# Optimization experiments

Hardware: AMD Instinct MI355X
Metric: run time of the kernel (lower is better)

The kernel has to match this reference:

```python
import jax, jax.numpy as jnp
import numpy as np

BS, Hq, Wq = 4, 64, 64
C, M, K, L = 256, 8, 4, 4
CV = C // M
SCALES = [(64, 64), (32, 32), (16, 16), (8, 8)]


def grid_sample_nhwc(img, grid):
    """torch.F.grid_sample(mode='bilinear', padding_mode='zeros', align_corners=False).
    img: [N,h,w,Cf], grid: [N,H,W,2] with (x,y) in [-1,1]. Returns [N,H,W,Cf]."""
    N, h, w, _ = img.shape
    x = (grid[..., 0] + 1.0) * (w * 0.5) - 0.5
    y = (grid[..., 1] + 1.0) * (h * 0.5) - 0.5
    x0 = jnp.floor(x)
    y0 = jnp.floor(y)
    wx1 = x - x0
    wy1 = y - y0
    wx0 = 1.0 - wx1
    wy0 = 1.0 - wy1
    b = jnp.arange(N)[:, None, None]

    def gather(yi, xi):
        valid = ((xi >= 0) & (xi < w) & (yi >= 0) & (yi < h)).astype(img.dtype)
        xi_c = jnp.clip(xi, 0, w - 1).astype(jnp.int32)
        yi_c = jnp.clip(yi, 0, h - 1).astype(jnp.int32)
        return img[b, yi_c, xi_c] * valid[..., None]  # [N,H,W,Cf]

    return (gather(y0, x0) * (wy0 * wx0)[..., None]
            + gather(y0, x0 + 1.0) * (wy0 * wx1)[..., None]
            + gather(y0 + 1.0, x0) * (wy1 * wx0)[..., None]
            + gather(y0 + 1.0, x0 + 1.0) * (wy1 * wx1)[..., None])


def _forward(q, feats, ref, Wz, bz, Wo, bo, Wa, ba, Wp, bp, Wm, bm):
    BM = BS * M
    z = q @ Wz + bz  # [BS,H,W,C]
    # learned offsets: [BS,H,W,2MKL] -> [BS,M,L,K,H,W,2] -> [BM,L,K,H,W,2]
    off = (z @ Wo + bo).reshape(BS, Hq, Wq, M, L, K, 2)
    off = off.transpose(0, 3, 4, 5, 1, 2, 6).reshape(BM, L, K, Hq, Wq, 2)
    # attention weights over the L*K samples per head
    attn = jax.nn.softmax((z @ Wa + ba).reshape(BS, Hq, Wq, M, L * K), axis=-1)
    attn = attn.transpose(0, 3, 1, 2, 4).reshape(BM, Hq * Wq, L * K)

    samples = []
    for l, f in enumerate(feats):
        h, w = f.shape[1], f.shape[2]
        # value projection, split heads: [BS,h,w,C] -> [BM,h,w,CV] (BS outer, M inner)
        wp = (f @ Wp + bp).reshape(BS, h, w, M, CV).transpose(0, 3, 1, 2, 4).reshape(BM, h, w, CV)
        # phi(h,w,ref) then .repeat(M,1,1,1): tile with M as the OUTER axis (faithful to source)
        pref = jnp.stack([ref[..., 0] * (w - 1), ref[..., 1] * (h - 1)], axis=-1)  # [BS,H,W,2]
        pref = jnp.tile(pref, (M, 1, 1, 1))  # [BM,H,W,2]
        pts = pref[:, None] + off[:, l]  # [BM,K,H,W,2]
        gx = 2.0 * pts[..., 0] / max(w - 1, 1) - 1.0
        gy = 2.0 * pts[..., 1] / max(h - 1, 1) - 1.0
        grid = jnp.stack([gx, gy], axis=-1)  # [BM,K,H,W,2]
        s = jax.vmap(grid_sample_nhwc, in_axes=(None, 1), out_axes=0)(wp, grid)  # [K,BM,H,W,CV]
        samples.append(s.transpose(1, 4, 2, 0, 3))  # [BM,CV,H,K,W] == torch.stack(..., dim=3)

    sf = jnp.stack(samples, axis=1)  # [BM,L,CV,H,K,W]
    # faithful to source: permute(0,4,5,3,1,2) then raw view to [BM, H*W, CV, L*K]
    sf = sf.transpose(0, 4, 5, 3, 1, 2).reshape(BM, Hq * Wq, CV, L * K)
    out = jnp.einsum('nlds,nls->nld', sf, attn)  # [BM,HW,CV]
    out = out.reshape(BS, M, Hq, Wq, CV).transpose(0, 2, 3, 1, 4).reshape(BS, Hq, Wq, C)
    return out @ Wm + bm


def setup_inputs() -> dict:
    key = jax.random.key(0)
    ks = jax.random.split(key, 12)
    s = 0.02
    inp = {
        'q': jax.random.normal(ks[0], (BS, Hq, Wq, C), jnp.float32),
        'ref': jax.random.uniform(ks[1], (BS, Hq, Wq, 2), jnp.float32),
    }
    for i, (h, w) in enumerate(SCALES):
        inp[f'feat{i}'] = jax.random.normal(jax.random.fold_in(ks[2], i), (BS, h, w, C), jnp.float32)
    inp['Wz'] = jax.random.normal(ks[3], (C, C), jnp.float32) * s
    inp['bz'] = jnp.zeros((C,), jnp.float32)
    inp['Wo'] = jax.random.normal(ks[4], (C, 2 * M * K * L), jnp.float32) * s
    inp['bo'] = jnp.zeros((2 * M * K * L,), jnp.float32)
    inp['Wa'] = jax.random.normal(ks[5], (C, M * K * L), jnp.float32) * s
    inp['ba'] = jnp.zeros((M * K * L,), jnp.float32)
    inp['Wp'] = jax.random.normal(ks[6], (C, C), jnp.float32) * s
    inp['bp'] = jnp.zeros((C,), jnp.float32)
    inp['Wm'] = jax.random.normal(ks[7], (C, C), jnp.float32) * s
    inp['bm'] = jnp.zeros((C,), jnp.float32)
    return inp


def reference(q, feat0, feat1, feat2, feat3, ref, Wz, bz, Wo, bo, Wa, ba, Wp, bp, Wm, bm):
    return _forward(q, [feat0, feat1, feat2, feat3], ref, Wz, bz, Wo, bo, Wa, ba, Wp, bp, Wm, bm)
```

## Files before the change

### kernel.cpp

```cpp
#include <hip/hip_runtime.h>
#include <hip/hip_bf16.h>


typedef __attribute__((ext_vector_type(8))) _Float16 half8;
typedef __attribute__((ext_vector_type(2))) _Float16 half2t;
typedef __attribute__((ext_vector_type(4))) float f32x4;

#if __has_builtin(__builtin_amdgcn_fdot2)
__device__ __forceinline__ float fdot2f(half2t a, half2t b, float c) {
    return __builtin_amdgcn_fdot2(a, b, c, false);
}
#else
__device__ __forceinline__ float fdot2f(half2t a, half2t b, float c) {
    return c + (float)a.x * (float)b.x + (float)a.y * (float)b.y;
}
#endif

#define GLOAD_LDS16(gp, lp)                                                      \
    __builtin_amdgcn_global_load_lds(                                            \
        (const __attribute__((address_space(1))) void*)(gp),                     \
        (__attribute__((address_space(3))) void*)(lp), 16, 0, 0)

__device__ __forceinline__ int swz(int row, int sem_q) {
    return row * 32 + ((sem_q ^ (row & 3)) * 8);
}

__global__ __launch_bounds__(256) void transpose_w(
    const float* __restrict__ Wz, const float* __restrict__ Wo,
    const float* __restrict__ Wa, const float* __restrict__ Wp,
    const float* __restrict__ Wm,
    _Float16* __restrict__ Wzt, _Float16* __restrict__ Woat,
    _Float16* __restrict__ Wpt, _Float16* __restrict__ Wmt)
{
    __shared__ float ts[64][65];
    const int bid = blockIdx.x;
    const float* src; _Float16* dst; int N, tile;
    if      (bid < 16) { src = Wz; dst = Wzt;          N = 256; tile = bid; }
    else if (bid < 32) { src = Wo; dst = Woat;         N = 256; tile = bid - 16; }
    else if (bid < 40) { src = Wa; dst = Woat + 65536; N = 128; tile = bid - 32; }
    else if (bid < 56) { src = Wp; dst = Wpt;          N = 256; tile = bid - 40; }
    else               { src = Wm; dst = Wmt;          N = 256; tile = bid - 56; }
    const int ntn = N >> 6;
    const int k0 = (tile / ntn) * 64, n0 = (tile % ntn) * 64;
    const int t = threadIdx.x, tx = t & 63, ty = t >> 6;
    #pragma unroll
    for (int r = 0; r < 16; ++r) {
        const int kk = r * 4 + ty;
        ts[kk][tx] = src[(size_t)(k0 + kk) * N + n0 + tx];
    }
    __syncthreads();
    #pragma unroll
    for (int r = 0; r < 16; ++r) {
        const int nn = r * 4 + ty;
        dst[(size_t)(n0 + nn) * 256 + k0 + tx] = (_Float16)ts[tx][nn];
    }
}

template<typename AT>
__device__ __forceinline__ void gemm_core(
    _Float16* __restrict__ As, _Float16* __restrict__ Bs,
    const AT* __restrict__ A, const _Float16* __restrict__ Bt,
    int m0, int n0, f32x4 (&acc)[4][4])
{
    const int t    = threadIdx.x;
    const int lane = t & 63, wid = t >> 6;
    const int wr = wid >> 1, wc = wid & 1;
    const int lr = lane & 15, sq = lane >> 4;

    const int grow = lane >> 2;
    const int gqs  = (lane & 3) ^ ((lane >> 2) & 3);

    for (int kt = 0; kt < 256; kt += 32) {
        if constexpr (sizeof(AT) == 4) {
            const int arow = t >> 1, ac = t & 1;
            const float* ap = (const float*)A + (size_t)(m0 + arow) * 256 + kt + ac * 16;
            float v[16];
            #pragma unroll
            for (int i = 0; i < 4; ++i) {
                float4 f = ((const float4*)ap)[i];
                v[4*i] = f.x; v[4*i+1] = f.y; v[4*i+2] = f.z; v[4*i+3] = f.w;
            }
            half8 h0, h1;
            #pragma unroll
            for (int i = 0; i < 8; ++i) { h0[i] = (_Float16)v[i]; h1[i] = (_Float16)v[8+i]; }
            *(half8*)&As[swz(arow, ac * 2)]     = h0;
            *(half8*)&As[swz(arow, ac * 2 + 1)] = h1;
        } else {
            #pragma unroll
            for (int h = 0; h < 2; ++h) {
                const int rbase = wid * 32 + h * 16;
                const _Float16* ga = (const _Float16*)A +
                    (size_t)(m0 + rbase + grow) * 256 + kt + gqs * 8;
                GLOAD_LDS16(ga, &As[rbase * 32]);
            }
        }
        #pragma unroll
        for (int h = 0; h < 2; ++h) {
            const int rbase = wid * 32 + h * 16;
            const _Float16* gb = Bt +
                (size_t)(n0 + rbase + grow) * 256 + kt + gqs * 8;
            GLOAD_LDS16(gb, &Bs[rbase * 32]);
        }
        __syncthreads();

        half8 af[4], bf[4];
        #pragma unroll
        for (int m = 0; m < 4; ++m)
            af[m] = *(const half8*)&As[swz(wr*64 + m*16 + lr, sq)];
        #pragma unroll
        for (int n = 0; n < 4; ++n)
            bf[n] = *(const half8*)&Bs[swz(wc*64 + n*16 + lr, sq)];
        #pragma unroll
        for (int m = 0; m < 4; ++m)
            #pragma unroll
            for (int n = 0; n < 4; ++n)
                acc[m][n] = __builtin_amdgcn_mfma_f32_16x16x32_f16(af[m], bf[n], acc[m][n], 0, 0, 0);
        __syncthreads();
    }
}

__device__ __forceinline__ void epi_f16(
    f32x4 (&acc)[4][4], const float* __restrict__ bias,
    _Float16* __restrict__ C, int N, int m0, int n0)
{
    const int t = threadIdx.x, lane = t & 63, wid = t >> 6;
    const int wr = wid >> 1, wc = wid & 1, lr = lane & 15;
    #pragma unroll
    for (int n = 0; n < 4; ++n) {
        const int col = n0 + wc*64 + n*16 + lr;
        const float bv = bias[col];
        #pragma unroll
        for (int m = 0; m < 4; ++m)
            #pragma unroll
            for (int r = 0; r < 4; ++r) {
                const int row = m0 + wr*64 + m*16 + (lane >> 4)*4 + r;
                C[(size_t)row * N + col] = (_Float16)(acc[m][n][r] + bv);
            }
    }
}

__device__ __forceinline__ void epi_wp(
    f32x4 (&acc)[4][4], const float* __restrict__ bias,
    _Float16* __restrict__ C, int m0, int n0, int shift)
{
    const int t = threadIdx.x, lane = t & 63, wid = t >> 6;
    const int wr = wid >> 1, wc = wid & 1, lr = lane & 15;
    const int mask = (1 << shift) - 1;
    #pragma unroll
    for (int n = 0; n < 4; ++n) {
        const int col = n0 + wc*64 + n*16 + lr;
        const float bv = bias[col];
        const int mh = col >> 5, cv = col & 31;
        #pragma unroll
        for (int m = 0; m < 4; ++m)
            #pragma unroll
            for (int r = 0; r < 4; ++r) {
                const int row = m0 + wr*64 + m*16 + (lane >> 4)*4 + r;
                const int bb = row >> shift, pix = row & mask;
                C[((((size_t)(bb * 8 + mh)) << shift) + pix) * 32 + cv] =
                    (_Float16)(acc[m][n][r] + bv);
            }
    }
}

__global__ __launch_bounds__(256) void gemm_z_wp(
    const float* __restrict__ q, const _Float16* __restrict__ Wzt,
    const float* __restrict__ bz, _Float16* __restrict__ z,
    const float* __restrict__ f0, const float* __restrict__ f1,
    const float* __restrict__ f2, const float* __restrict__ f3,
    const _Float16* __restrict__ Wpt, const float* __restrict__ bp,
    _Float16* __restrict__ w0, _Float16* __restrict__ w1,
    _Float16* __restrict__ w2, _Float16* __restrict__ w3)
{
    __shared__ _Float16 As[128 * 32];
    __shared__ _Float16 Bs[128 * 32];
    const int by = blockIdx.y, bx = blockIdx.x;
    f32x4 acc[4][4] = {};
    if (by < 128) {
        gemm_core<float>(As, Bs, q, Wzt, by * 128, bx * 128, acc);
        epi_f16(acc, bz, z, 256, by * 128, bx * 128);
    } else {
        const int y = by - 128;
        const float* A; _Float16* C; int m0, shift;
        if      (y < 128) { A = f0; C = w0; m0 = y * 128;         shift = 12; }
        else if (y < 160) { A = f1; C = w1; m0 = (y - 128) * 128; shift = 10; }
        else if (y < 168) { A = f2; C = w2; m0 = (y - 160) * 128; shift = 8;  }
        else              { A = f3; C = w3; m0 = (y - 168) * 128; shift = 6;  }
        gemm_core<float>(As, Bs, A, Wpt, m0, bx * 128, acc);
        epi_wp(acc, bp, C, m0, bx * 128, shift);
    }
}

__global__ __launch_bounds__(256) void gemm_zo_at(
    const _Float16* __restrict__ z, const _Float16* __restrict__ Woat,
    const float* __restrict__ bo, const float* __restrict__ ba,
    _Float16* __restrict__ zo, _Float16* __restrict__ attn)
{
    __shared__ __align__(16) char ldsbuf[128 * 136 * 2];
    _Float16* As = (_Float16*)ldsbuf;
    _Float16* Bs = As + 128 * 32;
    _Float16 (*smax)[136] = (_Float16(*)[136])ldsbuf;

    const int bx = blockIdx.x, by = blockIdx.y;
    const int m0 = by * 128;
    f32x4 acc[4][4] = {};
    gemm_core<_Float16>(As, Bs, z, Woat, m0, bx * 128, acc);

    const int t = threadIdx.x, lane = t & 63, wid = t >> 6;
    const int wr = wid >> 1, wc = wid & 1, lr = lane & 15;

    if (bx < 2) {
        #pragma unroll
        for (int n = 0; n < 4; ++n) {
            const int c = bx * 128 + wc*64 + n*16 + lr;
            const float bv = bo[c];
            const int cp = (((c >> 3) & 3) << 6) | ((c >> 5) << 3)
                         | (((c >> 1) & 3) << 1) | (c & 1);
            #pragma unroll
            for (int m = 0; m < 4; ++m)
                #pragma unroll
                for (int r = 0; r < 4; ++r) {
                    const int row = m0 + wr*64 + m*16 + (lane >> 4)*4 + r;
                    zo[(size_t)row * 256 + cp] = (_Float16)(acc[m][n][r] + bv);
                }
        }
    } else {
        __syncthreads();
        #pragma unroll
        for (int n = 0; n < 4; ++n) {
            const int col = wc*64 + n*16 + lr;
            const float bv = ba[col];
            #pragma unroll
            for (int m = 0; m < 4; ++m)
                #pragma unroll
                for (int r = 0; r < 4; ++r) {
                    const int rowl = wr*64 + m*16 + (lane >> 4)*4 + r;
                    smax[rowl][col] = (_Float16)(acc[m][n][r] + bv);
                }
        }
        __syncthreads();
        #pragma unroll
        for (int j = 0; j < 4; ++j) {
            const int g    = j * 256 + t;
            const int rowl = g >> 3, mh = g & 7;
            const half8* sp = (const half8*)&smax[rowl][mh * 16];
            const half8 a = sp[0], bb8 = sp[1];
            float v[16];
            #pragma unroll
            for (int i = 0; i < 8; ++i) { v[i] = (float)a[i]; v[8+i] = (float)bb8[i]; }
            float mx = v[0];
            #pragma unroll
            for (int i = 1; i < 16; ++i) mx = fmaxf(mx, v[i]);
            float s = 0.f;
            #pragma unroll
            for (int i = 0; i < 16; ++i) { v[i] = expf(v[i] - mx); s += v[i]; }
            const float inv = 1.f / s;
            half8 o0, o1;
            #pragma unroll
            for (int i = 0; i < 8; ++i) { o0[i] = (_Float16)(v[i]*inv); o1[i] = (_Float16)(v[8+i]*inv); }
            const int row  = m0 + rowl;
            const int qpos = row & 4095, b = row >> 12;
            const int k = qpos >> 10, qx = (qpos >> 4) & 63, ya = qpos & 15;
            half8* op = (half8*)(attn +
                ((((((size_t)b * 64 + qx) * 16 + ya) * 8 + mh) * 4 + k) * 16));
            op[0] = o0; op[1] = o1;
        }
    }
}

__global__ __launch_bounds__(256) void sample8(
    const _Float16* __restrict__ zo,
    const _Float16* __restrict__ attn,
    const float* __restrict__ ref,
    const _Float16* __restrict__ wp0, const _Float16* __restrict__ wp1,
    const _Float16* __restrict__ wp2, const _Float16* __restrict__ wp3,
    _Float16* __restrict__ outp)
{
    const int bid = blockIdx.x;
    const int bp_ = (bid & 7) * 1024 + (bid >> 3);
    const int t  = threadIdx.x;
    const int k  = t & 3;
    const int m  = (t >> 2) & 7;
    const int qp = (t >> 5) & 1;
    const int l  = t >> 6;

    const int query = bp_ * 2 + qp;
    const int qx = query & 63;
    const int qy = (query >> 6) & 63;
    const int b  = query >> 12;

    const int ya = qy >> 2, yb = qy & 3;
    const int p  = (k << 10) | (qx << 4) | ya;
    const int cb = m * 32 + yb * 8 + l * 2;

    const int hw = 64 >> l;
    const int shift = 12 - 2 * l;
    const float fw = (float)hw;
    const _Float16* wp = (l == 0) ? wp0 : (l == 1) ? wp1 : (l == 2) ? wp2 : wp3;

    const unsigned off2 = *(const unsigned*)(zo + (size_t)query * 256 + (l * 64 + m * 8 + k * 2));
    const half2t offh = __builtin_bit_cast(half2t, off2);
    const float offx = (float)offh.x;
    const float offy = (float)offh.y;

    const int rb = m & 3;
    const float2 rr = *(const float2*)(ref + ((size_t)(rb * 4096) + qy * 64 + qx) * 2);

    const float px  = rr.x * (fw - 1.f) + offx;
    const float py  = rr.y * (fw - 1.f) + offy;
    const float gx  = 2.f * px / (fw - 1.f) - 1.f;
    const float gy  = 2.f * py / (fw - 1.f) - 1.f;
    const float xim = (gx + 1.f) * (fw * 0.5f) - 0.5f;
    const float yim = (gy + 1.f) * (fw * 0.5f) - 0.5f;

    const float x0f = floorf(xim), y0f = floorf(yim);
    const float wx1 = xim - x0f, wy1 = yim - y0f;
    const float wx0 = 1.f - wx1, wy0 = 1.f - wy1;
    const int ix0 = (int)x0f, iy0 = (int)y0f;

    half2t w[8];
    {
        const uint4* ap = (const uint4*)(attn +
            ((((((size_t)b * 64 + qx) * 16 + ya) * 8 + m) * 4 + k) * 16));
        const uint4 wa = ap[0], wb = ap[1];
        w[0] = __builtin_bit_cast(half2t, wa.x); w[1] = __builtin_bit_cast(half2t, wa.y);
        w[2] = __builtin_bit_cast(half2t, wa.z); w[3] = __builtin_bit_cast(half2t, wa.w);
        w[4] = __builtin_bit_cast(half2t, wb.x); w[5] = __builtin_bit_cast(half2t, wb.y);
        w[6] = __builtin_bit_cast(half2t, wb.z); w[7] = __builtin_bit_cast(half2t, wb.w);
    }

    const _Float16* plane = wp + ((((size_t)(b * 8 + m)) << shift) * 32);

    float r0 = 0.f, r1 = 0.f;
    #pragma unroll
    for (int tap = 0; tap < 4; ++tap) {
        int iy = iy0 + (tap >> 1);
        int ix = ix0 + (tap & 1);
        const bool ok = (iy >= 0) & (iy < hw) & (ix >= 0) & (ix < hw);
        float wt = ((tap >> 1) ? wy1 : wy0) * ((tap & 1) ? wx1 : wx0);
        wt = ok ? wt : 0.f;
        iy = min(max(iy, 0), hw - 1);
        ix = min(max(ix, 0), hw - 1);
        const uint4* tp = (const uint4*)(plane + ((size_t)(iy * hw + ix)) * 32);
        const uint4 u0 = tp[0], u1 = tp[1], u2 = tp[2], u3 = tp[3];
        float d0 = 0.f, d1 = 0.f;
        d0 = fdot2f(__builtin_bit_cast(half2t, u0.x), w[0], d0);
        d0 = fdot2f(__builtin_bit_cast(half2t, u0.y), w[1], d0);
        d0 = fdot2f(__builtin_bit_cast(half2t, u0.z), w[2], d0);
        d0 = fdot2f(__builtin_bit_cast(half2t, u0.w), w[3], d0);
        d0 = fdot2f(__builtin_bit_cast(half2t, u1.x), w[4], d0);
        d0 = fdot2f(__builtin_bit_cast(half2t, u1.y), w[5], d0);
        d0 = fdot2f(__builtin_bit_cast(half2t, u1.z), w[6], d0);
        d0 = fdot2f(__builtin_bit_cast(half2t, u1.w), w[7], d0);
        d1 = fdot2f(__builtin_bit_cast(half2t, u2.x), w[0], d1);
        d1 = fdot2f(__builtin_bit_cast(half2t, u2.y), w[1], d1);
        d1 = fdot2f(__builtin_bit_cast(half2t, u2.z), w[2], d1);
        d1 = fdot2f(__builtin_bit_cast(half2t, u2.w), w[3], d1);
        d1 = fdot2f(__builtin_bit_cast(half2t, u3.x), w[4], d1);
        d1 = fdot2f(__builtin_bit_cast(half2t, u3.y), w[5], d1);
        d1 = fdot2f(__builtin_bit_cast(half2t, u3.z), w[6], d1);
        d1 = fdot2f(__builtin_bit_cast(half2t, u3.w), w[7], d1);
        r0 += wt * d0;
        r1 += wt * d1;
    }

    half2t o; o.x = (_Float16)r0; o.y = (_Float16)r1;
    *(half2t*)(outp + ((size_t)b * 4096 + p) * 256 + cb) = o;
}

__global__ __launch_bounds__(256) void gemm_final(
    const _Float16* __restrict__ A, const _Float16* __restrict__ Wmt,
    const float* __restrict__ bias, float* __restrict__ C)
{
    __shared__ _Float16 As[128 * 32];
    __shared__ _Float16 Bs[128 * 32];
    const int m0 = blockIdx.y * 128, n0 = blockIdx.x * 128;
    f32x4 acc[4][4] = {};
    gemm_core<_Float16>(As, Bs, A, Wmt, m0, n0, acc);
    const int t = threadIdx.x, lane = t & 63, wid = t >> 6;
    const int wr = wid >> 1, wc = wid & 1, lr = lane & 15;
    #pragma unroll
    for (int n = 0; n < 4; ++n) {
        const int col = n0 + wc*64 + n*16 + lr;
        const float bv = bias[col];
        #pragma unroll
        for (int m = 0; m < 4; ++m)
            #pragma unroll
            for (int r = 0; r < 4; ++r) {
                const int row = m0 + wr*64 + m*16 + (lane >> 4)*4 + r;
                C[(size_t)row * 256 + col] = acc[m][n][r] + bv;
            }
    }
}

extern "C" void kernel_launch(void* const* d_in, const int* in_sizes, int n_in,
                              void* d_out, int out_size, void* d_ws, size_t ws_size,
                              hipStream_t stream)
{
    const float* q   = (const float*)d_in[0];
    const float* ref = (const float*)d_in[1];
    const float* f0  = (const float*)d_in[2];
    const float* f1  = (const float*)d_in[3];
    const float* f2  = (const float*)d_in[4];
    const float* f3  = (const float*)d_in[5];
    const float* Wz  = (const float*)d_in[6];
    const float* bz  = (const float*)d_in[7];
    const float* Wo  = (const float*)d_in[8];
    const float* bo  = (const float*)d_in[9];
    const float* Wa  = (const float*)d_in[10];
    const float* ba  = (const float*)d_in[11];
    const float* Wp  = (const float*)d_in[12];
    const float* bp  = (const float*)d_in[13];
    const float* Wm  = (const float*)d_in[14];
    const float* bm  = (const float*)d_in[15];
    float* out = (float*)d_out;

    char* ws = (char*)d_ws;
    _Float16* z    = (_Float16*)(ws + ((size_t)0));
    _Float16* zo   = (_Float16*)(ws + ((size_t)16 << 20));
    _Float16* attn = (_Float16*)(ws + ((size_t)24 << 20));
    _Float16* wp0  = (_Float16*)(ws + ((size_t)28 << 20));
    _Float16* wp1  = (_Float16*)(ws + ((size_t)36 << 20));
    _Float16* wp2  = (_Float16*)(ws + ((size_t)38 << 20));
    _Float16* wp3  = (_Float16*)(ws + ((size_t)38 << 20) + ((size_t)512 << 10));
    _Float16* Wzt  = (_Float16*)(ws + ((size_t)40 << 20));
    _Float16* Woat = (_Float16*)(ws + ((size_t)40 << 20) + ((size_t)256 << 10));
    _Float16* Wpt  = (_Float16*)(ws + ((size_t)40 << 20) + ((size_t)768 << 10));
    _Float16* Wmt  = (_Float16*)(ws + ((size_t)41 << 20));
    _Float16* outp = z;

    const dim3 blk(256);

    transpose_w<<<dim3(72), blk, 0, stream>>>(Wz, Wo, Wa, Wp, Wm, Wzt, Woat, Wpt, Wmt);
    gemm_z_wp<<<dim3(2, 298), blk, 0, stream>>>(q, Wzt, bz, z,
                                                f0, f1, f2, f3, Wpt, bp,
                                                wp0, wp1, wp2, wp3);
    gemm_zo_at<<<dim3(3, 128), blk, 0, stream>>>(z, Woat, bo, ba, zo, attn);
    sample8<<<dim3(8192), blk, 0, stream>>>(zo, attn, ref, wp0, wp1, wp2, wp3, outp);
    gemm_final<<<dim3(2, 128), blk, 0, stream>>>(outp, Wmt, bm, out);
}
```

Baseline: 90.19 us.

## Widen GEMM tiles to full 256-column N so each A row-tile is loaded once

The GEMM core is templated on the number of N repeats, and the z/Wp projection and final GEMMs now use 128x256 tiles covering the whole output width in one block. This halves the grid for those kernels, so the fp32 A operand (q, feats, sampled output) is read and converted once instead of twice. In exchange each thread holds twice the accumulators (128 floats), which raises register pressure, lowers occupancy and leaves fewer blocks to fill the GPU.

```diff
diff --git a/kernel.cpp b/kernel.cpp
--- a/kernel.cpp
+++ b/kernel.cpp
@@ -56,11 +56,11 @@
     }
 }
 
-template<typename AT>
-__device__ __forceinline__ void gemm_core(
+template<typename AT, int NREP>
+__device__ __forceinline__ void gemm_coreN(
     _Float16* __restrict__ As, _Float16* __restrict__ Bs,
     const AT* __restrict__ A, const _Float16* __restrict__ Bt,
-    int m0, int n0, f32x4 (&acc)[4][4])
+    int m0, int n0, f32x4 (&acc)[4][NREP])
 {
     const int t    = threadIdx.x;
     const int lane = t & 63, wid = t >> 6;
@@ -95,39 +95,40 @@
             }
         }
         #pragma unroll
-        for (int h = 0; h < 2; ++h) {
-            const int rbase = wid * 32 + h * 16;
+        for (int h = 0; h < NREP / 2; ++h) {
+            const int rbase = wid * (NREP * 8) + h * 16;
             const _Float16* gb = Bt +
                 (size_t)(n0 + rbase + grow) * 256 + kt + gqs * 8;
             GLOAD_LDS16(gb, &Bs[rbase * 32]);
         }
         __syncthreads();
 
-        half8 af[4], bf[4];
+        half8 af[4], bf[NREP];
         #pragma unroll
         for (int m = 0; m < 4; ++m)
             af[m] = *(const half8*)&As[swz(wr*64 + m*16 + lr, sq)];
         #pragma unroll
-        for (int n = 0; n < 4; ++n)
-            bf[n] = *(const half8*)&Bs[swz(wc*64 + n*16 + lr, sq)];
+        for (int n = 0; n < NREP; ++n)
+            bf[n] = *(const half8*)&Bs[swz(wc*(NREP*16) + n*16 + lr, sq)];
         #pragma unroll
         for (int m = 0; m < 4; ++m)
             #pragma unroll
-            for (int n = 0; n < 4; ++n)
+            for (int n = 0; n < NREP; ++n)
                 acc[m][n] = __builtin_amdgcn_mfma_f32_16x16x32_f16(af[m], bf[n], acc[m][n], 0, 0, 0);
         __syncthreads();
     }
 }
 
-__device__ __forceinline__ void epi_f16(
-    f32x4 (&acc)[4][4], const float* __restrict__ bias,
+template<int NREP>
+__device__ __forceinline__ void epi_f16N(
+    f32x4 (&acc)[4][NREP], const float* __restrict__ bias,
     _Float16* __restrict__ C, int N, int m0, int n0)
 {
     const int t = threadIdx.x, lane = t & 63, wid = t >> 6;
     const int wr = wid >> 1, wc = wid & 1, lr = lane & 15;
     #pragma unroll
-    for (int n = 0; n < 4; ++n) {
-        const int col = n0 + wc*64 + n*16 + lr;
+    for (int n = 0; n < NREP; ++n) {
+        const int col = n0 + wc*(NREP*16) + n*16 + lr;
         const float bv = bias[col];
         #pragma unroll
         for (int m = 0; m < 4; ++m)
@@ -139,16 +140,17 @@
     }
 }
 
-__device__ __forceinline__ void epi_wp(
-    f32x4 (&acc)[4][4], const float* __restrict__ bias,
+template<int NREP>
+__device__ __forceinline__ void epi_wpN(
+    f32x4 (&acc)[4][NREP], const float* __restrict__ bias,
     _Float16* __restrict__ C, int m0, int n0, int shift)
 {
     const int t = threadIdx.x, lane = t & 63, wid = t >> 6;
     const int wr = wid >> 1, wc = wid & 1, lr = lane & 15;
     const int mask = (1 << shift) - 1;
     #pragma unroll
-    for (int n = 0; n < 4; ++n) {
-        const int col = n0 + wc*64 + n*16 + lr;
+    for (int n = 0; n < NREP; ++n) {
+        const int col = n0 + wc*(NREP*16) + n*16 + lr;
         const float bv = bias[col];
         const int mh = col >> 5, cv = col & 31;
         #pragma unroll
@@ -173,12 +175,12 @@
     _Float16* __restrict__ w2, _Float16* __restrict__ w3)
 {
     __shared__ _Float16 As[128 * 32];
-    __shared__ _Float16 Bs[128 * 32];
-    const int by = blockIdx.y, bx = blockIdx.x;
-    f32x4 acc[4][4] = {};
+    __shared__ _Float16 Bs[256 * 32];
+    const int by = blockIdx.y;
+    f32x4 acc[4][8] = {};
     if (by < 128) {
-        gemm_core<float>(As, Bs, q, Wzt, by * 128, bx * 128, acc);
-        epi_f16(acc, bz, z, 256, by * 128, bx * 128);
+        gemm_coreN<float, 8>(As, Bs, q, Wzt, by * 128, 0, acc);
+        epi_f16N<8>(acc, bz, z, 256, by * 128, 0);
     } else {
         const int y = by - 128;
         const float* A; _Float16* C; int m0, shift;
@@ -186,8 +188,8 @@
         else if (y < 160) { A = f1; C = w1; m0 = (y - 128) * 128; shift = 10; }
         else if (y < 168) { A = f2; C = w2; m0 = (y - 160) * 128; shift = 8;  }
         else              { A = f3; C = w3; m0 = (y - 168) * 128; shift = 6;  }
-        gemm_core<float>(As, Bs, A, Wpt, m0, bx * 128, acc);
-        epi_wp(acc, bp, C, m0, bx * 128, shift);
+        gemm_coreN<float, 8>(As, Bs, A, Wpt, m0, 0, acc);
+        epi_wpN<8>(acc, bp, C, m0, 0, shift);
     }
 }
 
@@ -204,7 +206,7 @@
     const int bx = blockIdx.x, by = blockIdx.y;
     const int m0 = by * 128;
     f32x4 acc[4][4] = {};
-    gemm_core<_Float16>(As, Bs, z, Woat, m0, bx * 128, acc);
+    gemm_coreN<_Float16, 4>(As, Bs, z, Woat, m0, bx * 128, acc);
 
     const int t = threadIdx.x, lane = t & 63, wid = t >> 6;
     const int wr = wid >> 1, wc = wid & 1, lr = lane & 15;
@@ -373,15 +375,15 @@
     const float* __restrict__ bias, float* __restrict__ C)
 {
     __shared__ _Float16 As[128 * 32];
-    __shared__ _Float16 Bs[128 * 32];
-    const int m0 = blockIdx.y * 128, n0 = blockIdx.x * 128;
-    f32x4 acc[4][4] = {};
-    gemm_core<_Float16>(As, Bs, A, Wmt, m0, n0, acc);
+    __shared__ _Float16 Bs[256 * 32];
+    const int m0 = blockIdx.y * 128;
+    f32x4 acc[4][8] = {};
+    gemm_coreN<_Float16, 8>(As, Bs, A, Wmt, m0, 0, acc);
     const int t = threadIdx.x, lane = t & 63, wid = t >> 6;
     const int wr = wid >> 1, wc = wid & 1, lr = lane & 15;
     #pragma unroll
-    for (int n = 0; n < 4; ++n) {
-        const int col = n0 + wc*64 + n*16 + lr;
+    for (int n = 0; n < 8; ++n) {
+        const int col = wc*128 + n*16 + lr;
         const float bv = bias[col];
         #pragma unroll
         for (int m = 0; m < 4; ++m)
@@ -432,10 +434,10 @@
     const dim3 blk(256);
 
     transpose_w<<<dim3(72), blk, 0, stream>>>(Wz, Wo, Wa, Wp, Wm, Wzt, Woat, Wpt, Wmt);
-    gemm_z_wp<<<dim3(2, 298), blk, 0, stream>>>(q, Wzt, bz, z,
+    gemm_z_wp<<<dim3(1, 298), blk, 0, stream>>>(q, Wzt, bz, z,
                                                 f0, f1, f2, f3, Wpt, bp,
                                                 wp0, wp1, wp2, wp3);
     gemm_zo_at<<<dim3(3, 128), blk, 0, stream>>>(z, Woat, bo, ba, zo, attn);
     sample8<<<dim3(8192), blk, 0, stream>>>(zo, attn, ref, wp0, wp1, wp2, wp3, outp);
-    gemm_final<<<dim3(2, 128), blk, 0, stream>>>(outp, Wmt, bm, out);
-}
+    gemm_final<<<dim3(1, 128), blk, 0, stream>>>(outp, Wmt, bm, out);
+}
```

New measurement: 98.01 us. 1.09x slower.
